# Optimization experiments

Measured on AMD Instinct MI355X. Metric: run time of the kernel, lower is better.

The kernel has to match this reference:

```python
import jax, jax.numpy as jnp
import numpy as np

EMB_SIZE = 768
BLOCK_SIZE = 64
NUM_CLASS = 97
N = 4096
NUM_BLOCKS = EMB_SIZE // BLOCK_SIZE  # 12


def setup_inputs() -> dict:
    key = jax.random.key(0)
    k1, k2, k3 = jax.random.split(key, 3)
    head_embeddings = jax.random.normal(k1, (N, EMB_SIZE), dtype=jnp.float32)
    tail_embeddings = jax.random.normal(k2, (N, EMB_SIZE), dtype=jnp.float32)
    # xavier_uniform for [NUM_CLASS, EMB_SIZE*BLOCK_SIZE]
    fan_in = EMB_SIZE * BLOCK_SIZE
    fan_out = NUM_CLASS
    bound = float(np.sqrt(6.0 / (fan_in + fan_out)))
    W = jax.random.uniform(k3, (NUM_CLASS, EMB_SIZE * BLOCK_SIZE), dtype=jnp.float32,
                           minval=-bound, maxval=bound)
    b = jnp.full((NUM_CLASS,), 0.1, dtype=jnp.float32)
    return {"head_embeddings": head_embeddings, "tail_embeddings": tail_embeddings,
            "W": W, "b": b}


def reference(head_embeddings, tail_embeddings, W, b):
    n = head_embeddings.shape[0]
    b1 = head_embeddings.reshape(n, NUM_BLOCKS, BLOCK_SIZE)  # [N, K, S]
    b2 = tail_embeddings.reshape(n, NUM_BLOCKS, BLOCK_SIZE)  # [N, K, S]
    # block-wise outer product: [N, K, S, S] -> [N, K*S*S]
    bl = jnp.einsum('nki,nkj->nkij', b1, b2).reshape(n, EMB_SIZE * BLOCK_SIZE)
    logits = bl @ W.T + b  # [N, NUM_CLASS]
    return logits
```

## Files before the change

### kernel.cpp

```cpp
#include <hip/hip_runtime.h>
#include <hip/hip_bf16.h>
#include <stdint.h>

#define NROWS 4096
#define NCLS  97
#define EMB   768
#define KTOT  49152
#define OUT_ELEMS (NROWS * NCLS)
#define E_ELEMS  (NROWS * EMB)
#define NK32  (KTOT / 32)
#define WT_BYTES ((size_t)NK32 * 128 * 64)
#define EB_BYTES ((size_t)E_ELEMS * 2)

typedef __attribute__((ext_vector_type(8)))  short short8;
typedef __attribute__((ext_vector_type(4)))  float floatx4;
typedef __bf16 bf16x2 __attribute__((ext_vector_type(2)));
typedef __bf16 bf16x8 __attribute__((ext_vector_type(8)));

__device__ __forceinline__ uint32_t pkmul(uint32_t a, uint32_t b) {
  bf16x2 x = __builtin_bit_cast(bf16x2, a);
  bf16x2 y = __builtin_bit_cast(bf16x2, b);
  bf16x2 r = x * y;
  return __builtin_bit_cast(uint32_t, r);
}

__device__ __forceinline__ uint4 cvt8(float4 a, float4 b) {
  bf16x8 v;
  v[0] = (__bf16)a.x; v[1] = (__bf16)a.y; v[2] = (__bf16)a.z; v[3] = (__bf16)a.w;
  v[4] = (__bf16)b.x; v[5] = (__bf16)b.y; v[6] = (__bf16)b.z; v[7] = (__bf16)b.w;
  return __builtin_bit_cast(uint4, v);
}

__global__ void prep(const float* __restrict__ W,
                     const float* __restrict__ b1,
                     const float* __restrict__ b2,
                     uint4* __restrict__ wt,
                     uint4* __restrict__ b1b,
                     uint4* __restrict__ b2b,
                     int nmax)
{
  const int nwt = NK32 * 128 * 4;
  const int nE8 = E_ELEMS / 8;
  int t = blockIdx.x * blockDim.x + threadIdx.x;
  if (t >= nmax) return;
  if (t < nwt) {
    int eo = t & 3;
    int c  = (t >> 2) & 127;
    int kc = t >> 9;
    uint4 v = uint4{0u, 0u, 0u, 0u};
    if (c < NCLS) {
      const float4* p = (const float4*)(W + (size_t)c * KTOT + kc * 32 + eo * 8);
      v = cvt8(p[0], p[1]);
    }
    wt[t] = v;
  } else if (t < nwt + nE8) {
    int i = t - nwt;
    const float4* p = (const float4*)b1 + (size_t)2 * i;
    b1b[i] = cvt8(p[0], p[1]);
  } else {
    int i = t - nwt - nE8;
    const float4* p = (const float4*)b2 + (size_t)2 * i;
    b2b[i] = cvt8(p[0], p[1]);
  }
}

template<bool BMIR>
__global__ __launch_bounds__(256, 2)
void bilinear_main(const void* __restrict__ b1p,
                   const void* __restrict__ b2p,
                   const char* __restrict__ Wt,
                   const float* __restrict__ biasg,
                   float* __restrict__ P,
                   float* __restrict__ outd,
                   int klen)
{
  const int tid  = threadIdx.x;
  const int w    = tid >> 6;
  const int l    = tid & 63;
  const int l15  = l & 15;
  const int quad = l >> 4;
  const int mhalf = w & 1;
  const int chalf = w >> 1;
  const bool cfull = (chalf == 0);
  const int bm = blockIdx.y;
  const int k0 = blockIdx.x * klen;

  int nrow[4];
#pragma unroll
  for (int rt = 0; rt < 4; ++rt) nrow[rt] = bm * 128 + mhalf * 64 + rt * 16 + l15;

  const char* wtl = Wt + (size_t)(k0 >> 5) * 8192
                       + (chalf * 64 + l15) * 64 + quad * 16;

  floatx4 acc[4][4];
#pragma unroll
  for (int rt = 0; rt < 4; ++rt)
#pragma unroll
    for (int ct = 0; ct < 4; ++ct)
      acc[rt][ct] = floatx4{0.f, 0.f, 0.f, 0.f};

  uint4 b2c[4][2];
  uint4 b1c[4];
  int cur_k = -1;
  const int nwin = klen >> 6;

  for (int gwin = 0; gwin < nwin; gwin += 8) {
    const int kap0 = k0 + (gwin << 6);
    const int kblk = kap0 >> 12;
    const int i0   = (kap0 >> 6) & 63;
    if (kblk != cur_k) {
      cur_k = kblk;
#pragma unroll
      for (int rt = 0; rt < 4; ++rt)
#pragma unroll
        for (int kh = 0; kh < 2; ++kh) {
          if (BMIR) {
            b2c[rt][kh] = *(const uint4*)((const char*)b2p +
                            (size_t)nrow[rt] * 1536 + kblk * 128 + kh * 64 + quad * 16);
          } else {
            const float* p = (const float*)b2p + (size_t)nrow[rt] * EMB +
                             kblk * 64 + kh * 32 + quad * 8;
            b2c[rt][kh] = cvt8(((const float4*)p)[0], ((const float4*)p)[1]);
          }
        }
    }
#pragma unroll
    for (int rt = 0; rt < 4; ++rt) {
      if (BMIR) {
        b1c[rt] = *(const uint4*)((const char*)b1p +
                     (size_t)nrow[rt] * 1536 + kblk * 128 + i0 * 2);
      } else {
        const float* p = (const float*)b1p + (size_t)nrow[rt] * EMB + kblk * 64 + i0;
        b1c[rt] = cvt8(((const float4*)p)[0], ((const float4*)p)[1]);
      }
    }

#pragma unroll
    for (int ii = 0; ii < 8; ++ii) {
      const char* pw = wtl + (size_t)(gwin + ii) * 16384;

      uint32_t s2[4];
#pragma unroll
      for (int rt = 0; rt < 4; ++rt) {
        uint32_t d = (&b1c[rt].x)[ii >> 1];
        uint32_t h = (ii & 1) ? (d >> 16) : (d & 0xffffu);
        s2[rt] = h | (h << 16);
      }

#pragma unroll
      for (int kh = 0; kh < 2; ++kh) {
        short8 wf[4];
#pragma unroll
        for (int ct = 0; ct < 4; ++ct)
          if (ct < 3 || cfull)
            wf[ct] = __builtin_bit_cast(short8,
                       *(const uint4*)(pw + kh * 8192 + ct * 1024));
        uint4 afr[4];
#pragma unroll
        for (int rt = 0; rt < 4; ++rt) {
          afr[rt].x = pkmul(s2[rt], b2c[rt][kh].x);
          afr[rt].y = pkmul(s2[rt], b2c[rt][kh].y);
          afr[rt].z = pkmul(s2[rt], b2c[rt][kh].z);
          afr[rt].w = pkmul(s2[rt], b2c[rt][kh].w);
        }
#pragma unroll
        for (int rt = 0; rt < 4; ++rt) {
          short8 af = __builtin_bit_cast(short8, afr[rt]);
#pragma unroll
          for (int ct = 0; ct < 4; ++ct)
            if (ct < 3 || cfull)
              acc[rt][ct] = __builtin_amdgcn_mfma_f32_16x16x32_bf16(
                                af, wf[ct], acc[rt][ct], 0, 0, 0);
        }
      }
    }
  }

  if (P) {
    float* Pb = P + (size_t)blockIdx.x * OUT_ELEMS;
#pragma unroll
    for (int rt = 0; rt < 4; ++rt)
#pragma unroll
      for (int ct = 0; ct < 4; ++ct) {
        const int c = chalf * 64 + ct * 16 + l15;
        if (c < NCLS) {
#pragma unroll
          for (int r = 0; r < 4; ++r) {
            const int row = bm * 128 + mhalf * 64 + rt * 16 + quad * 4 + r;
            Pb[(size_t)row * NCLS + c] = acc[rt][ct][r];
          }
        }
      }
  } else {
#pragma unroll
    for (int rt = 0; rt < 4; ++rt)
#pragma unroll
      for (int ct = 0; ct < 4; ++ct) {
        const int c = chalf * 64 + ct * 16 + l15;
        if (c < NCLS) {
          const float bv = biasg[c];
#pragma unroll
          for (int r = 0; r < 4; ++r) {
            const int row = bm * 128 + mhalf * 64 + rt * 16 + quad * 4 + r;
            outd[(size_t)row * NCLS + c] = acc[rt][ct][r] + bv;
          }
        }
      }
  }
}

template<int KSC>
__global__ void reduce_bias_t(const float* __restrict__ P,
                              const float* __restrict__ biasg,
                              float* __restrict__ out)
{
  int i = blockIdx.x * blockDim.x + threadIdx.x;
  const int n4 = OUT_ELEMS / 4;
  if (i >= n4) return;
  int c0 = (i * 4) % NCLS;
  int c1 = c0 + 1 == NCLS ? 0 : c0 + 1;
  int c2 = c1 + 1 == NCLS ? 0 : c1 + 1;
  int c3 = c2 + 1 == NCLS ? 0 : c2 + 1;
  float4 s;
  s.x = biasg[c0]; s.y = biasg[c1]; s.z = biasg[c2]; s.w = biasg[c3];
  const float4* P4 = (const float4*)P;
#pragma unroll
  for (int t = 0; t < KSC; ++t) {
    float4 v = P4[(size_t)t * n4 + i];
    s.x += v.x; s.y += v.y; s.z += v.z; s.w += v.w;
  }
  ((float4*)out)[i] = s;
}

static void launch_reduce(int KS, const float* P, const float* bb, float* out,
                          hipStream_t stream) {
  const int nb = (OUT_ELEMS / 4 + 255) / 256;
  switch (KS) {
    case 32: reduce_bias_t<32><<<nb, 256, 0, stream>>>(P, bb, out); break;
    case 24: reduce_bias_t<24><<<nb, 256, 0, stream>>>(P, bb, out); break;
    case 16: reduce_bias_t<16><<<nb, 256, 0, stream>>>(P, bb, out); break;
    case 12: reduce_bias_t<12><<<nb, 256, 0, stream>>>(P, bb, out); break;
    case 8:  reduce_bias_t<8><<<nb, 256, 0, stream>>>(P, bb, out);  break;
    case 6:  reduce_bias_t<6><<<nb, 256, 0, stream>>>(P, bb, out);  break;
    case 4:  reduce_bias_t<4><<<nb, 256, 0, stream>>>(P, bb, out);  break;
    case 3:  reduce_bias_t<3><<<nb, 256, 0, stream>>>(P, bb, out);  break;
    case 2:  reduce_bias_t<2><<<nb, 256, 0, stream>>>(P, bb, out);  break;
    default: reduce_bias_t<1><<<nb, 256, 0, stream>>>(P, bb, out);  break;
  }
}

extern "C" void kernel_launch(void* const* d_in, const int* in_sizes, int n_in,
                              void* d_out, int out_size, void* d_ws, size_t ws_size,
                              hipStream_t stream) {
  const float* b1f = (const float*)d_in[0];
  const float* b2f = (const float*)d_in[1];
  const float* Wf  = (const float*)d_in[2];
  const float* bbf = (const float*)d_in[3];
  float* out = (float*)d_out;

  const size_t resv_full = WT_BYTES + 2 * EB_BYTES;
  const size_t slice     = (size_t)OUT_ELEMS * 4;
  static const int cands[] = {32, 24, 16, 12, 8, 6, 4, 3, 2, 1};
  const int NC = 10;

  int KS = 0; bool bmir = false;
  for (int i = 0; i < NC; ++i)
    if (resv_full + (size_t)cands[i] * slice <= ws_size) { KS = cands[i]; bmir = true; break; }
  if (!bmir)
    for (int i = 0; i < NC; ++i)
      if (WT_BYTES + (size_t)cands[i] * slice <= ws_size) { KS = cands[i]; break; }

  uint4* Wt  = (uint4*)d_ws;
  uint4* b1b = (uint4*)((char*)d_ws + WT_BYTES);
  uint4* b2b = (uint4*)((char*)d_ws + WT_BYTES + EB_BYTES);
  const int nwt = NK32 * 128 * 4;
  const int nE8 = E_ELEMS / 8;
  const int nprep = bmir ? (nwt + 2 * nE8) : nwt;

  prep<<<(nprep + 255) / 256, 256, 0, stream>>>(Wf, b1f, b2f, Wt, b1b, b2b, nprep);

  if (KS > 0) {
    float* P = (float*)((char*)d_ws + (bmir ? resv_full : WT_BYTES));
    if (bmir)
      bilinear_main<true><<<dim3(KS, 32), 256, 0, stream>>>(
          (const void*)b1b, (const void*)b2b, (const char*)Wt, bbf, P, nullptr, KTOT / KS);
    else
      bilinear_main<false><<<dim3(KS, 32), 256, 0, stream>>>(
          (const void*)b1f, (const void*)b2f, (const char*)Wt, bbf, P, nullptr, KTOT / KS);
    launch_reduce(KS, P, bbf, out, stream);
  } else {
    bilinear_main<false><<<dim3(1, 32), 256, 0, stream>>>(
        (const void*)b1f, (const void*)b2f, (const char*)Wt, bbf, nullptr, out, KTOT);
  }
}
```

Baseline: 160.7 us.

## Drop bf16 embedding mirrors; form outer-product in fp32 and cap K-split at 16

The prep kernel no longer converts the head and tail embeddings to bf16. The main kernel instead keeps the tail block in fp32 registers and multiplies it by the fp32 head scalar before converting each product to bf16 for the MFMA. This removes a prep pass and its workspace, and rounds the product only once instead of twice. In exchange it adds many fp32 multiplies and conversions in the inner loop and more register pressure from 64 floats of b2 per thread. The K-split candidates 32 and 24 are removed, so the grid now has at most 16 split blocks along K.

Result: faster. 152.8 us (-4.9%).

```diff
diff --git a/kernel.cpp b/kernel.cpp
--- a/kernel.cpp
+++ b/kernel.cpp
@@ -10,19 +10,11 @@
 #define E_ELEMS  (NROWS * EMB)
 #define NK32  (KTOT / 32)
 #define WT_BYTES ((size_t)NK32 * 128 * 64)
-#define EB_BYTES ((size_t)E_ELEMS * 2)
 
 typedef __attribute__((ext_vector_type(8)))  short short8;
 typedef __attribute__((ext_vector_type(4)))  float floatx4;
 typedef __bf16 bf16x2 __attribute__((ext_vector_type(2)));
 typedef __bf16 bf16x8 __attribute__((ext_vector_type(8)));
-
-__device__ __forceinline__ uint32_t pkmul(uint32_t a, uint32_t b) {
-  bf16x2 x = __builtin_bit_cast(bf16x2, a);
-  bf16x2 y = __builtin_bit_cast(bf16x2, b);
-  bf16x2 r = x * y;
-  return __builtin_bit_cast(uint32_t, r);
-}
 
 __device__ __forceinline__ uint4 cvt8(float4 a, float4 b) {
   bf16x8 v;
@@ -31,43 +23,30 @@
   return __builtin_bit_cast(uint4, v);
 }
 
-__global__ void prep(const float* __restrict__ W,
-                     const float* __restrict__ b1,
-                     const float* __restrict__ b2,
-                     uint4* __restrict__ wt,
-                     uint4* __restrict__ b1b,
-                     uint4* __restrict__ b2b,
-                     int nmax)
+__device__ __forceinline__ uint32_t mkbf2(float lo, float hi) {
+  bf16x2 v; v[0] = (__bf16)lo; v[1] = (__bf16)hi;
+  return __builtin_bit_cast(uint32_t, v);
+}
+
+__global__ void prep(const float* __restrict__ W, uint4* __restrict__ wt)
 {
   const int nwt = NK32 * 128 * 4;
-  const int nE8 = E_ELEMS / 8;
   int t = blockIdx.x * blockDim.x + threadIdx.x;
-  if (t >= nmax) return;
-  if (t < nwt) {
-    int eo = t & 3;
-    int c  = (t >> 2) & 127;
-    int kc = t >> 9;
-    uint4 v = uint4{0u, 0u, 0u, 0u};
-    if (c < NCLS) {
-      const float4* p = (const float4*)(W + (size_t)c * KTOT + kc * 32 + eo * 8);
-      v = cvt8(p[0], p[1]);
-    }
-    wt[t] = v;
-  } else if (t < nwt + nE8) {
-    int i = t - nwt;
-    const float4* p = (const float4*)b1 + (size_t)2 * i;
-    b1b[i] = cvt8(p[0], p[1]);
-  } else {
-    int i = t - nwt - nE8;
-    const float4* p = (const float4*)b2 + (size_t)2 * i;
-    b2b[i] = cvt8(p[0], p[1]);
-  }
-}
-
-template<bool BMIR>
+  if (t >= nwt) return;
+  int eo = t & 3;
+  int c  = (t >> 2) & 127;
+  int kc = t >> 9;
+  uint4 v = uint4{0u, 0u, 0u, 0u};
+  if (c < NCLS) {
+    const float4* p = (const float4*)(W + (size_t)c * KTOT + kc * 32 + eo * 8);
+    v = cvt8(p[0], p[1]);
+  }
+  wt[t] = v;
+}
+
 __global__ __launch_bounds__(256, 2)
-void bilinear_main(const void* __restrict__ b1p,
-                   const void* __restrict__ b2p,
+void bilinear_main(const float* __restrict__ b1f,
+                   const float* __restrict__ b2f,
                    const char* __restrict__ Wt,
                    const float* __restrict__ biasg,
                    float* __restrict__ P,
@@ -99,8 +78,7 @@
     for (int ct = 0; ct < 4; ++ct)
       acc[rt][ct] = floatx4{0.f, 0.f, 0.f, 0.f};
 
-  uint4 b2c[4][2];
-  uint4 b1c[4];
+  float b2r[4][2][8];
   int cur_k = -1;
   const int nwin = klen >> 6;
 
@@ -114,63 +92,56 @@
       for (int rt = 0; rt < 4; ++rt)
 #pragma unroll
         for (int kh = 0; kh < 2; ++kh) {
-          if (BMIR) {
-            b2c[rt][kh] = *(const uint4*)((const char*)b2p +
-                            (size_t)nrow[rt] * 1536 + kblk * 128 + kh * 64 + quad * 16);
-          } else {
-            const float* p = (const float*)b2p + (size_t)nrow[rt] * EMB +
-                             kblk * 64 + kh * 32 + quad * 8;
-            b2c[rt][kh] = cvt8(((const float4*)p)[0], ((const float4*)p)[1]);
-          }
+          const float* p = b2f + (size_t)nrow[rt] * EMB + kblk * 64 + kh * 32 + quad * 8;
+          float4 v0 = ((const float4*)p)[0];
+          float4 v1 = ((const float4*)p)[1];
+          b2r[rt][kh][0] = v0.x; b2r[rt][kh][1] = v0.y;
+          b2r[rt][kh][2] = v0.z; b2r[rt][kh][3] = v0.w;
+          b2r[rt][kh][4] = v1.x; b2r[rt][kh][5] = v1.y;
+          b2r[rt][kh][6] = v1.z; b2r[rt][kh][7] = v1.w;
         }
     }
-#pragma unroll
-    for (int rt = 0; rt < 4; ++rt) {
-      if (BMIR) {
-        b1c[rt] = *(const uint4*)((const char*)b1p +
-                     (size_t)nrow[rt] * 1536 + kblk * 128 + i0 * 2);
-      } else {
-        const float* p = (const float*)b1p + (size_t)nrow[rt] * EMB + kblk * 64 + i0;
-        b1c[rt] = cvt8(((const float4*)p)[0], ((const float4*)p)[1]);
-      }
-    }
-
-#pragma unroll
-    for (int ii = 0; ii < 8; ++ii) {
-      const char* pw = wtl + (size_t)(gwin + ii) * 16384;
-
-      uint32_t s2[4];
-#pragma unroll
-      for (int rt = 0; rt < 4; ++rt) {
-        uint32_t d = (&b1c[rt].x)[ii >> 1];
-        uint32_t h = (ii & 1) ? (d >> 16) : (d & 0xffffu);
-        s2[rt] = h | (h << 16);
-      }
-
-#pragma unroll
-      for (int kh = 0; kh < 2; ++kh) {
-        short8 wf[4];
-#pragma unroll
-        for (int ct = 0; ct < 4; ++ct)
-          if (ct < 3 || cfull)
-            wf[ct] = __builtin_bit_cast(short8,
-                       *(const uint4*)(pw + kh * 8192 + ct * 1024));
-        uint4 afr[4];
-#pragma unroll
-        for (int rt = 0; rt < 4; ++rt) {
-          afr[rt].x = pkmul(s2[rt], b2c[rt][kh].x);
-          afr[rt].y = pkmul(s2[rt], b2c[rt][kh].y);
-          afr[rt].z = pkmul(s2[rt], b2c[rt][kh].z);
-          afr[rt].w = pkmul(s2[rt], b2c[rt][kh].w);
-        }
-#pragma unroll
-        for (int rt = 0; rt < 4; ++rt) {
-          short8 af = __builtin_bit_cast(short8, afr[rt]);
+
+#pragma unroll
+    for (int ih = 0; ih < 2; ++ih) {
+      float4 b1v[4];
+#pragma unroll
+      for (int rt = 0; rt < 4; ++rt)
+        b1v[rt] = *(const float4*)(b1f + (size_t)nrow[rt] * EMB +
+                                   kblk * 64 + i0 + ih * 4);
+
+#pragma unroll
+      for (int ii2 = 0; ii2 < 4; ++ii2) {
+        const int iw = gwin + ih * 4 + ii2;
+        const char* pw = wtl + (size_t)iw * 16384;
+
+        float s[4];
+#pragma unroll
+        for (int rt = 0; rt < 4; ++rt)
+          s[rt] = (&b1v[rt].x)[ii2];
+
+#pragma unroll
+        for (int kh = 0; kh < 2; ++kh) {
+          short8 wf[4];
 #pragma unroll
           for (int ct = 0; ct < 4; ++ct)
             if (ct < 3 || cfull)
-              acc[rt][ct] = __builtin_amdgcn_mfma_f32_16x16x32_bf16(
-                                af, wf[ct], acc[rt][ct], 0, 0, 0);
+              wf[ct] = __builtin_bit_cast(short8,
+                         *(const uint4*)(pw + kh * 8192 + ct * 1024));
+#pragma unroll
+          for (int rt = 0; rt < 4; ++rt) {
+            uint4 afr;
+            afr.x = mkbf2(b2r[rt][kh][0] * s[rt], b2r[rt][kh][1] * s[rt]);
+            afr.y = mkbf2(b2r[rt][kh][2] * s[rt], b2r[rt][kh][3] * s[rt]);
+            afr.z = mkbf2(b2r[rt][kh][4] * s[rt], b2r[rt][kh][5] * s[rt]);
+            afr.w = mkbf2(b2r[rt][kh][6] * s[rt], b2r[rt][kh][7] * s[rt]);
+            short8 af = __builtin_bit_cast(short8, afr);
+#pragma unroll
+            for (int ct = 0; ct < 4; ++ct)
+              if (ct < 3 || cfull)
+                acc[rt][ct] = __builtin_amdgcn_mfma_f32_16x16x32_bf16(
+                                  af, wf[ct], acc[rt][ct], 0, 0, 0);
+          }
         }
       }
     }
@@ -236,8 +207,6 @@
                           hipStream_t stream) {
   const int nb = (OUT_ELEMS / 4 + 255) / 256;
   switch (KS) {
-    case 32: reduce_bias_t<32><<<nb, 256, 0, stream>>>(P, bb, out); break;
-    case 24: reduce_bias_t<24><<<nb, 256, 0, stream>>>(P, bb, out); break;
     case 16: reduce_bias_t<16><<<nb, 256, 0, stream>>>(P, bb, out); break;
     case 12: reduce_bias_t<12><<<nb, 256, 0, stream>>>(P, bb, out); break;
     case 8:  reduce_bias_t<8><<<nb, 256, 0, stream>>>(P, bb, out);  break;
@@ -258,38 +227,26 @@
   const float* bbf = (const float*)d_in[3];
   float* out = (float*)d_out;
 
-  const size_t resv_full = WT_BYTES + 2 * EB_BYTES;
-  const size_t slice     = (size_t)OUT_ELEMS * 4;
-  static const int cands[] = {32, 24, 16, 12, 8, 6, 4, 3, 2, 1};
-  const int NC = 10;
-
-  int KS = 0; bool bmir = false;
+  const size_t slice = (size_t)OUT_ELEMS * 4;
+  static const int cands[] = {16, 12, 8, 6, 4, 3, 2, 1};
+  const int NC = 8;
+
+  int KS = 0;
   for (int i = 0; i < NC; ++i)
-    if (resv_full + (size_t)cands[i] * slice <= ws_size) { KS = cands[i]; bmir = true; break; }
-  if (!bmir)
-    for (int i = 0; i < NC; ++i)
-      if (WT_BYTES + (size_t)cands[i] * slice <= ws_size) { KS = cands[i]; break; }
-
-  uint4* Wt  = (uint4*)d_ws;
-  uint4* b1b = (uint4*)((char*)d_ws + WT_BYTES);
-  uint4* b2b = (uint4*)((char*)d_ws + WT_BYTES + EB_BYTES);
+    if (WT_BYTES + (size_t)cands[i] * slice <= ws_size) { KS = cands[i]; break; }
+
+  uint4* Wt = (uint4*)d_ws;
   const int nwt = NK32 * 128 * 4;
-  const int nE8 = E_ELEMS / 8;
-  const int nprep = bmir ? (nwt + 2 * nE8) : nwt;
-
-  prep<<<(nprep + 255) / 256, 256, 0, stream>>>(Wf, b1f, b2f, Wt, b1b, b2b, nprep);
+
+  prep<<<(nwt + 255) / 256, 256, 0, stream>>>(Wf, Wt);
 
   if (KS > 0) {
-    float* P = (float*)((char*)d_ws + (bmir ? resv_full : WT_BYTES));
-    if (bmir)
-      bilinear_main<true><<<dim3(KS, 32), 256, 0, stream>>>(
-          (const void*)b1b, (const void*)b2b, (const char*)Wt, bbf, P, nullptr, KTOT / KS);
-    else
-      bilinear_main<false><<<dim3(KS, 32), 256, 0, stream>>>(
-          (const void*)b1f, (const void*)b2f, (const char*)Wt, bbf, P, nullptr, KTOT / KS);
+    float* P = (float*)((char*)d_ws + WT_BYTES);
+    bilinear_main<<<dim3(KS, 32), 256, 0, stream>>>(
+        b1f, b2f, (const char*)Wt, bbf, P, nullptr, KTOT / KS);
     launch_reduce(KS, P, bbf, out, stream);
   } else {
-    bilinear_main<false><<<dim3(1, 32), 256, 0, stream>>>(
-        (const void*)b1f, (const void*)b2f, (const char*)Wt, bbf, nullptr, out, KTOT);
-  }
-}
+    bilinear_main<<<dim3(1, 32), 256, 0, stream>>>(
+        b1f, b2f, (const char*)Wt, bbf, nullptr, out, KTOT);
+  }
+}
```
